# Optimization experiments

Hardware: AMD Instinct MI355X
Metric: run time of the kernel (lower is better)

## Reference

```python
import jax, jax.numpy as jnp
from jax import lax
import numpy as np

EPS = 1e-5  # BatchNorm eps


def setup_inputs() -> dict:
    key = jax.random.key(0)
    ks = jax.random.split(key, 8)
    N, C_in, T, V = 64, 64, 300, 25
    C_out, K, KT = 64, 3, 9
    x = jax.random.normal(ks[0], (N, C_in, T, V), dtype=jnp.float32)
    A = jax.random.uniform(ks[1], (K, V, V), dtype=jnp.float32)
    # 1x1 conv weight squeezed to [K*C_out, C_in]
    w_gcn = jax.random.normal(ks[2], (K * C_out, C_in), dtype=jnp.float32) * (1.0 / np.sqrt(C_in))
    b_gcn = jax.random.normal(ks[3], (K * C_out,), dtype=jnp.float32) * 0.01
    # temporal conv weight [O, I, kT, 1]
    w_tcn = jax.random.normal(ks[4], (C_out, C_out, KT, 1), dtype=jnp.float32) * (1.0 / np.sqrt(C_out * KT))
    b_tcn = jax.random.normal(ks[5], (C_out,), dtype=jnp.float32) * 0.01
    gamma = jnp.ones((C_out,), dtype=jnp.float32)
    beta = jnp.zeros((C_out,), dtype=jnp.float32)
    return {"x": x, "A": A, "w_gcn": w_gcn, "b_gcn": b_gcn,
            "w_tcn": w_tcn, "b_tcn": b_tcn, "gamma": gamma, "beta": beta}


def reference(x, A, w_gcn, b_gcn, w_tcn, b_tcn, gamma, beta):
    K = A.shape[0]
    # unit_gcn: 1x1 conv (pointwise over channels) then spatial graph aggregation
    y = jnp.einsum('nctv,oc->notv', x, w_gcn) + b_gcn[None, :, None, None]  # [N, K*C, T, V]
    n, kc, t, v = y.shape
    y = y.reshape(n, K, kc // K, t, v)
    y = jnp.einsum('nkctv,kvw->nctw', y, A)  # [N, C, T, V]
    # unit_tcn: temporal conv (kernel 9x1, pad 4) + BatchNorm (training mode: batch stats)
    pad = (w_tcn.shape[2] - 1) // 2
    y = lax.conv_general_dilated(y, w_tcn, window_strides=(1, 1),
                                 padding=((pad, pad), (0, 0)),
                                 dimension_numbers=('NCHW', 'OIHW', 'NCHW'))
    y = y + b_tcn[None, :, None, None]
    mean = jnp.mean(y, axis=(0, 2, 3), keepdims=True)
    var = jnp.var(y, axis=(0, 2, 3), keepdims=True)
    y = (y - mean) * lax.rsqrt(var + EPS) * gamma[None, :, None, None] + beta[None, :, None, None]
    # residual (identity: in==out, stride==1) + ReLU
    return jax.nn.relu(y + x)
```

## Files before the change

### kernel.cpp

```cpp
#include <hip/hip_runtime.h>
#include <hip/hip_bf16.h>

#define N_    64
#define C_    64
#define T_    300
#define V_    25
#define K_    3
#define KT_   9
#define PAD_  4

typedef short bf16x8 __attribute__((ext_vector_type(8)));
typedef float f32x4  __attribute__((ext_vector_type(4)));

static __device__ __forceinline__ unsigned short f2bf(float f) {
    __hip_bfloat16 h = __float2bfloat16(f);
    return __builtin_bit_cast(unsigned short, h);
}
static __device__ __forceinline__ unsigned int pk2(float a, float b) {
    return (unsigned int)f2bf(a) | ((unsigned int)f2bf(b) << 16);
}
static __device__ __forceinline__ float bfhi(unsigned int u) {
    return __builtin_bit_cast(float, u << 16);
}
static __device__ __forceinline__ float bflo(unsigned int u) {
    return __builtin_bit_cast(float, u & 0xffff0000u);
}
static __device__ __forceinline__ float bf2f(unsigned short u) {
    return __builtin_bit_cast(float, (unsigned int)u << 16);
}

__global__ __launch_bounds__(256) void prep_kernel(
    const float* __restrict__ Wt, const float* __restrict__ Wg,
    const float* __restrict__ bg, const float* __restrict__ A,
    unsigned short* __restrict__ Wtb, unsigned short* __restrict__ Wgbt,
    unsigned short* __restrict__ bias2b, unsigned short* __restrict__ Abt)
{
    int i = blockIdx.x * 256 + threadIdx.x;
    if (i < 9*64*64) {
        int kt = i >> 12, r = i & 4095, o = r >> 6, c = r & 63;
        Wtb[i] = f2bf(Wt[(size_t)(o*64 + c)*9 + kt]);
    }
    int j = i - 9*64*64;
    if (j >= 0 && j < 64*192) {
        int o = j / 192, kc = j - 192*(j/192);
        int k = kc >> 6, ci = kc & 63;
        Wgbt[j] = f2bf(Wg[(size_t)(k*64 + o)*64 + ci]);
    }
    int m = j - 64*192;
    if (m >= 0 && m < 64*25) {
        int c = m / 25, w = m - 25*(m/25);
        float s = 0.f;
        for (int k = 0; k < 3; ++k) {
            float col = 0.f;
            for (int v = 0; v < 25; ++v) col += A[k*625 + v*25 + w];
            s += bg[k*64 + c] * col;
        }
        bias2b[w*64 + c] = f2bf(s);
    }
    int p = m - 64*25;
    if (p >= 0 && p < 3*32*40) {
        int k = p / 1280, r = p - 1280*k, w = r / 40, v = r - 40*(r/40);
        float val = (w < 25 && v < 25) ? A[k*625 + v*25 + w] : 0.f;
        Abt[p] = f2bf(val);
    }
}

#define GSUB   15
#define GGRP   (T_/GSUB)
#define NGBLK  (N_*GGRP)

__global__ __launch_bounds__(256, 5) void gcn_kernel(
    const float* __restrict__ x,
    const unsigned short* __restrict__ Wgbt,
    const unsigned short* __restrict__ Abt,
    const unsigned short* __restrict__ bias2b,
    unsigned short* __restrict__ y2)
{
    __shared__ unsigned short xslab[64*40];
    __shared__ unsigned short xa[32*200];
    __shared__ unsigned int   bias2L[25*34];

    const int tid  = threadIdx.x;
    const int n    = blockIdx.x / GGRP;
    const int tg   = (blockIdx.x % GGRP) * GSUB;
    const int lane = tid & 63, wave = tid >> 6;
    const int l15  = lane & 15, lq = lane >> 4;

    bf16x8 wfrag[6], afrag[6];
    #pragma unroll
    for (int cb = 0; cb < 6; ++cb) {
        wfrag[cb] = *(const bf16x8*)(Wgbt + (wave*16 + l15)*192 + cb*32 + lq*8);
        asm volatile("" : "+v"(wfrag[cb]));
    }
    #pragma unroll
    for (int s = 0; s < 6; ++s) {
        afrag[s] = *(const bf16x8*)(Abt + ((s >> 1)*32 + (s & 1)*16 + l15)*40 + lq*8);
        asm volatile("" : "+v"(afrag[s]));
    }

    for (int i = tid; i < 800; i += 256)
        bias2L[(i >> 5)*34 + (i & 31)] = ((const unsigned int*)bias2b)[i];
    if (tid < 192) {
        int r = tid / 3, z = tid - 3*(tid/3);
        ((unsigned int*)xslab)[r*20 + 13 + z] = 0u;
    }
    #pragma unroll
    for (int s = 0; s < 4; ++s) {
        int slot = tid + s*256;
        if (slot < 64*13) {
            int row = slot/13, sl = slot - 13*row;
            const float* xr = x + ((size_t)(n*C_ + row)*T_ + tg)*V_;
            float f0, f1;
            if (sl < 12) { float2 t2 = *(const float2*)(xr + 2*sl); f0 = t2.x; f1 = t2.y; }
            else         { f0 = xr[24]; f1 = 0.f; }
            ((unsigned int*)xslab)[row*20 + sl] = pk2(f0, f1);
        }
    }
    __syncthreads();

    for (int j = 0; j < GSUB; ++j) {
        const int t = tg + j;
        float2 Lr[4];
        const bool hn = (j + 1 < GSUB);
        if (hn) {
            #pragma unroll
            for (int s = 0; s < 4; ++s) {
                int slot = tid + s*256;
                if (slot < 64*13) {
                    int row = slot/13, sl = slot - 13*row;
                    const float* xr = x + ((size_t)(n*C_ + row)*T_ + t + 1)*V_;
                    if (sl < 12) Lr[s] = *(const float2*)(xr + 2*sl);
                    else         { Lr[s].x = xr[24]; Lr[s].y = 0.f; }
                }
            }
        }
        {
            bf16x8 xf = *(const bf16x8*)(xslab + (wave*16 + l15)*40 + lq*8);
            #pragma unroll
            for (int s = 0; s < 6; ++s) {
                f32x4 d = {};
                d = __builtin_amdgcn_mfma_f32_16x16x32_bf16(xf, afrag[s], d, 0, 0, 0);
                const int w = (s & 1)*16 + l15;
                if (w < 25) {
                    const int k = s >> 1;
                    unsigned long long pv = (unsigned long long)pk2(d[0], d[1])
                                          | ((unsigned long long)pk2(d[2], d[3]) << 32);
                    *(unsigned long long*)((char*)xa + w*400 + k*128 + wave*32 + lq*8) = pv;
                }
            }
        }
        __syncthreads();
        {
            f32x4 acc0 = {}, acc1 = {};
            #pragma unroll
            for (int cb = 0; cb < 6; ++cb) {
                bf16x8 b0 = *(const bf16x8*)((const char*)xa + l15*400      + cb*64 + lq*16);
                bf16x8 b1 = *(const bf16x8*)((const char*)xa + (16+l15)*400 + cb*64 + lq*16);
                acc0 = __builtin_amdgcn_mfma_f32_16x16x32_bf16(wfrag[cb], b0, acc0, 0, 0, 0);
                acc1 = __builtin_amdgcn_mfma_f32_16x16x32_bf16(wfrag[cb], b1, acc1, 0, 0, 0);
            }
            const int o0 = wave*16 + lq*4;
            {
                const int col = l15;
                unsigned int bu0 = bias2L[col*34 + (o0 >> 1)];
                unsigned int bu1 = bias2L[col*34 + (o0 >> 1) + 1];
                float v0 = acc0[0] + bfhi(bu0), v1 = acc0[1] + bflo(bu0);
                float v2 = acc0[2] + bfhi(bu1), v3 = acc0[3] + bflo(bu1);
                const size_t gcol = ((size_t)n*T_ + t)*V_ + col;
                *(unsigned long long*)(y2 + gcol*64 + o0) =
                      (unsigned long long)pk2(v0, v1)
                    | ((unsigned long long)pk2(v2, v3) << 32);
            }
            if (l15 < 9) {
                const int col = 16 + l15;
                unsigned int bu0 = bias2L[col*34 + (o0 >> 1)];
                unsigned int bu1 = bias2L[col*34 + (o0 >> 1) + 1];
                float v0 = acc1[0] + bfhi(bu0), v1 = acc1[1] + bflo(bu0);
                float v2 = acc1[2] + bfhi(bu1), v3 = acc1[3] + bflo(bu1);
                const size_t gcol = ((size_t)n*T_ + t)*V_ + col;
                *(unsigned long long*)(y2 + gcol*64 + o0) =
                      (unsigned long long)pk2(v0, v1)
                    | ((unsigned long long)pk2(v2, v3) << 32);
            }
        }
        if (hn) {
            #pragma unroll
            for (int s = 0; s < 4; ++s) {
                int slot = tid + s*256;
                if (slot < 64*13) {
                    int row = slot/13, sl = slot - 13*row;
                    ((unsigned int*)xslab)[row*20 + sl] = pk2(Lr[s].x, Lr[s].y);
                }
            }
        }
        __syncthreads();
    }
}

#define TTT    20
#define TCOLS  (TTT*25)
#define SLABC  712
#define TTILES (T_/TTT)
#define NBLK   (N_*TTILES)

#define TLOADA(dst, kt_) { \
    _Pragma("unroll") \
    for (int mt = 0; mt < 4; ++mt) \
        dst[mt] = *(const bf16x8*)(Wtb + (size_t)(kt_)*4096 + (mt*16 + l15)*64 \
                                   + h*32 + lq*8); }

#define TCOMP(a_, kt_) { \
    _Pragma("unroll") \
    for (int nf = 0; nf < 8; ++nf) { \
        int col = colw + nf*16 + l15 + (kt_)*25; \
        bf16x8 b = *(const bf16x8*)((const char*)slab + col*80 + lq*16); \
        _Pragma("unroll") \
        for (int mt = 0; mt < 4; ++mt) \
            acc[mt][nf] = __builtin_amdgcn_mfma_f32_16x16x32_bf16( \
                a_[mt], b, acc[mt][nf], 0, 0, 0); } }

template<int BF>
__global__ __launch_bounds__(256, 2) void tcn_kernel(
    const unsigned short* __restrict__ y2, const unsigned short* __restrict__ Wtb,
    const float* __restrict__ bt,
    unsigned short* __restrict__ y3b, float* __restrict__ y3f,
    float* __restrict__ psum, float* __restrict__ psq)
{
    __shared__ unsigned short slab[SLABC*40];
    __shared__ float s_sum[64], s_sq[64];

    const int tid = threadIdx.x;
    const int n  = blockIdx.x / TTILES;
    const int t0 = (blockIdx.x % TTILES) * TTT;
    const int lane = tid & 63, wave = tid >> 6;
    const int l15 = lane & 15, lq = lane >> 4;
    const int colw = wave * 128;

    if (tid < 64) { s_sum[tid] = 0.f; s_sq[tid] = 0.f; }

    f32x4 acc[4][8] = {};

    #pragma unroll
    for (int h = 0; h < 2; ++h) {
        __syncthreads();
        for (int i = tid; i < SLABC*4; i += 256) {
            int col = i >> 2, ck = i & 3;
            int tl = col / 25, v = col - 25*tl;
            int t = t0 - PAD_ + tl;
            float4 val = {0.f, 0.f, 0.f, 0.f};
            if (t >= 0 && t < T_)
                val = *(const float4*)(y2 + (((size_t)(n*T_ + t)*V_ + v)*64 + h*32 + ck*8));
            *(float4*)((char*)slab + col*80 + ck*16) = val;
        }
        __syncthreads();
        bf16x8 aA[4], aB[4];
        TLOADA(aA, 0);
        #pragma unroll
        for (int kt = 0; kt < 9; ++kt) {
            if ((kt & 1) == 0) {
                if (kt < 8) TLOADA(aB, kt + 1);
                TCOMP(aA, kt);
            } else {
                if (kt < 8) TLOADA(aA, kt + 1);
                TCOMP(aB, kt);
            }
        }
    }

    #pragma unroll
    for (int mt = 0; mt < 4; ++mt) {
        #pragma unroll
        for (int r = 0; r < 4; ++r) {
            const int o = mt*16 + lq*4 + r;
            const float bias = bt[o];
            float ls = 0.f, lsq = 0.f;
            #pragma unroll
            for (int nf = 0; nf < 8; ++nf) {
                int ocol = colw + nf*16 + l15;
                if (ocol < TCOLS) {
                    int tl = ocol / 25, v = ocol - 25*tl;
                    float val = acc[mt][nf][r] + bias;
                    size_t idx = ((size_t)(n*C_ + o)*T_ + t0 + tl)*V_ + v;
                    if (BF) y3b[idx] = f2bf(val);
                    else    y3f[idx] = val;
                    ls += val; lsq += val*val;
                }
            }
            atomicAdd(&s_sum[o], ls);
            atomicAdd(&s_sq[o], lsq);
        }
    }
    __syncthreads();
    if (tid < 64) {
        psum[(size_t)tid*NBLK + blockIdx.x] = s_sum[tid];
        psq [(size_t)tid*NBLK + blockIdx.x] = s_sq [tid];
    }
}

__global__ __launch_bounds__(256) void stats_kernel(
    const float* __restrict__ psum, const float* __restrict__ psq,
    const float* __restrict__ gamma, const float* __restrict__ beta,
    float* __restrict__ sb)
{
    const int o = blockIdx.x;
    const int tid = threadIdx.x;
    float s = 0.f, q = 0.f;
    for (int i = tid; i < NBLK; i += 256) {
        s += psum[(size_t)o*NBLK + i];
        q += psq [(size_t)o*NBLK + i];
    }
    __shared__ float rs[256], rq[256];
    rs[tid] = s; rq[tid] = q;
    __syncthreads();
    for (int off = 128; off > 0; off >>= 1) {
        if (tid < off) { rs[tid] += rs[tid + off]; rq[tid] += rq[tid + off]; }
        __syncthreads();
    }
    if (tid == 0) {
        const float cnt = (float)(N_ * T_ * V_);
        float mean = rs[0] / cnt;
        float var  = rq[0] / cnt - mean * mean;
        float rstd = rsqrtf(var + 1e-5f);
        float sc   = gamma[o] * rstd;
        sb[o]      = sc;
        sb[C_ + o] = beta[o] - mean * sc;
    }
}

__global__ __launch_bounds__(256) void bn_res_relu_bf16_kernel(
    const float* __restrict__ x, const unsigned short* __restrict__ y3b,
    const float* __restrict__ sb, float* __restrict__ out)
{
    const size_t total4 = (size_t)N_ * C_ * T_ * V_ / 4;
    size_t i4 = (size_t)blockIdx.x * 256 + threadIdx.x;
    if (i4 >= total4) return;
    const int c = (int)((i4 / (T_ * V_ / 4)) % C_);
    const float sc = sb[c], sh = sb[C_ + c];
    ushort4 yv = ((const ushort4*)y3b)[i4];
    float4 xv = ((const float4*)x)[i4];
    float4 o;
    o.x = fmaxf(bf2f(yv.x) * sc + sh + xv.x, 0.0f);
    o.y = fmaxf(bf2f(yv.y) * sc + sh + xv.y, 0.0f);
    o.z = fmaxf(bf2f(yv.z) * sc + sh + xv.z, 0.0f);
    o.w = fmaxf(bf2f(yv.w) * sc + sh + xv.w, 0.0f);
    ((float4*)out)[i4] = o;
}

__global__ __launch_bounds__(256) void bn_res_relu_f32_kernel(
    const float* __restrict__ x, const float* __restrict__ sb,
    float* __restrict__ y)
{
    const size_t total4 = (size_t)N_ * C_ * T_ * V_ / 4;
    size_t i4 = (size_t)blockIdx.x * 256 + threadIdx.x;
    if (i4 >= total4) return;
    const int c = (int)((i4 / (T_ * V_ / 4)) % C_);
    const float sc = sb[c], sh = sb[C_ + c];
    float4 yv = ((const float4*)y)[i4];
    float4 xv = ((const float4*)x)[i4];
    float4 o;
    o.x = fmaxf(yv.x * sc + sh + xv.x, 0.0f);
    o.y = fmaxf(yv.y * sc + sh + xv.y, 0.0f);
    o.z = fmaxf(yv.z * sc + sh + xv.z, 0.0f);
    o.w = fmaxf(yv.w * sc + sh + xv.w, 0.0f);
    ((float4*)y)[i4] = o;
}

extern "C" void kernel_launch(void* const* d_in, const int* in_sizes, int n_in,
                              void* d_out, int out_size, void* d_ws, size_t ws_size,
                              hipStream_t stream)
{
    const float* x     = (const float*)d_in[0];
    const float* A     = (const float*)d_in[1];
    const float* wg    = (const float*)d_in[2];
    const float* bg    = (const float*)d_in[3];
    const float* wt    = (const float*)d_in[4];
    const float* bt    = (const float*)d_in[5];
    const float* gamma = (const float*)d_in[6];
    const float* beta  = (const float*)d_in[7];
    float* out = (float*)d_out;

    char* wsb = (char*)d_ws;
    const size_t Y2B   = 61440000;
    const size_t Y3B   = 61440000;
    const size_t TABLE = 2*245760 + 512 + 73728 + 24576 + 3200 + 7680;
    const bool usebf = ws_size >= Y2B + Y3B + TABLE;

    unsigned short* y2  = (unsigned short*)wsb;
    unsigned short* y3b = (unsigned short*)(wsb + Y2B);
    const size_t base2  = usebf ? (Y2B + Y3B) : Y2B;
    float* psum            = (float*)(wsb + base2);
    float* psq             = (float*)(wsb + base2 + 245760);
    float* sb              = (float*)(wsb + base2 + 2*245760);
    unsigned short* Wtb    = (unsigned short*)(wsb + base2 + 2*245760 + 512);
    unsigned short* Wgbt   = (unsigned short*)(wsb + base2 + 2*245760 + 512 + 73728);
    unsigned short* bias2b = (unsigned short*)(wsb + base2 + 2*245760 + 512 + 73728 + 24576);
    unsigned short* Abt    = (unsigned short*)(wsb + base2 + 2*245760 + 512 + 73728 + 24576 + 3200);

    prep_kernel<<<214, 256, 0, stream>>>(wt, wg, bg, A, Wtb, Wgbt, bias2b, Abt);
    gcn_kernel<<<NGBLK, 256, 0, stream>>>(x, Wgbt, Abt, bias2b, y2);
    if (usebf)
        tcn_kernel<1><<<NBLK, 256, 0, stream>>>(y2, Wtb, bt, y3b, out, psum, psq);
    else
        tcn_kernel<0><<<NBLK, 256, 0, stream>>>(y2, Wtb, bt, y3b, out, psum, psq);
    stats_kernel<<<C_, 256, 0, stream>>>(psum, psq, gamma, beta, sb);
    const size_t total4 = (size_t)N_ * C_ * T_ * V_ / 4;
    const int bnblk = (int)((total4 + 255) / 256);
    if (usebf)
        bn_res_relu_bf16_kernel<<<bnblk, 256, 0, stream>>>(x, y3b, sb, out);
    else
        bn_res_relu_f32_kernel<<<bnblk, 256, 0, stream>>>(x, sb, out);
}
```

Measured before the change: 266.6 us.

## Widen tcn blocks to 8 waves and stage bf16 output through LDS

The temporal conv kernel now runs 512 threads, with each wave covering 64 output columns instead of 128, so the accumulator array is half as large and occupancy can rise. In the bf16 path, outputs are written into the shared slab and then copied to global memory as contiguous 32-bit words per channel row, replacing scattered 2-byte stores. The slab load loop also drops the per-element divide and time-bounds check in favour of a precomputed column range. The trade-offs are extra barriers and LDS traffic for the staging, and more threads competing for the same LDS.

```diff
diff --git a/kernel.cpp b/kernel.cpp
--- a/kernel.cpp
+++ b/kernel.cpp
@@ -202,6 +202,7 @@
 #define SLABC  712
 #define TTILES (T_/TTT)
 #define NBLK   (N_*TTILES)
+#define BBSTR  516
 
 #define TLOADA(dst, kt_) { \
     _Pragma("unroll") \
@@ -211,7 +212,7 @@
 
 #define TCOMP(a_, kt_) { \
     _Pragma("unroll") \
-    for (int nf = 0; nf < 8; ++nf) { \
+    for (int nf = 0; nf < 4; ++nf) { \
         int col = colw + nf*16 + l15 + (kt_)*25; \
         bf16x8 b = *(const bf16x8*)((const char*)slab + col*80 + lq*16); \
         _Pragma("unroll") \
@@ -220,7 +221,7 @@
                 a_[mt], b, acc[mt][nf], 0, 0, 0); } }
 
 template<int BF>
-__global__ __launch_bounds__(256, 2) void tcn_kernel(
+__global__ __launch_bounds__(512, 4) void tcn_kernel(
     const unsigned short* __restrict__ y2, const unsigned short* __restrict__ Wtb,
     const float* __restrict__ bt,
     unsigned short* __restrict__ y3b, float* __restrict__ y3f,
@@ -234,22 +235,24 @@
     const int t0 = (blockIdx.x % TTILES) * TTT;
     const int lane = tid & 63, wave = tid >> 6;
     const int l15 = lane & 15, lq = lane >> 4;
-    const int colw = wave * 128;
+    const int colw = wave * 64;
 
     if (tid < 64) { s_sum[tid] = 0.f; s_sq[tid] = 0.f; }
 
-    f32x4 acc[4][8] = {};
+    const int lo = (t0 < PAD_) ? (PAD_ - t0)*V_ : 0;
+    const int hi = (t0 + TTT + PAD_ > T_) ? (T_ + PAD_ - t0)*V_ : SLABC;
+
+    f32x4 acc[4][4] = {};
 
     #pragma unroll
     for (int h = 0; h < 2; ++h) {
         __syncthreads();
-        for (int i = tid; i < SLABC*4; i += 256) {
+        const long gbase = ((long)n*T_*V_ + (long)(t0 - PAD_)*V_)*64 + h*32;
+        for (int i = tid; i < SLABC*4; i += 512) {
             int col = i >> 2, ck = i & 3;
-            int tl = col / 25, v = col - 25*tl;
-            int t = t0 - PAD_ + tl;
             float4 val = {0.f, 0.f, 0.f, 0.f};
-            if (t >= 0 && t < T_)
-                val = *(const float4*)(y2 + (((size_t)(n*T_ + t)*V_ + v)*64 + h*32 + ck*8));
+            if (col >= lo && col < hi)
+                val = *(const float4*)(y2 + gbase + (long)col*64 + ck*8);
             *(float4*)((char*)slab + col*80 + ck*16) = val;
         }
         __syncthreads();
@@ -267,27 +270,65 @@
         }
     }
 
-    #pragma unroll
-    for (int mt = 0; mt < 4; ++mt) {
+    if (BF) {
+        unsigned short* bb = slab;
         #pragma unroll
-        for (int r = 0; r < 4; ++r) {
-            const int o = mt*16 + lq*4 + r;
-            const float bias = bt[o];
-            float ls = 0.f, lsq = 0.f;
-            #pragma unroll
-            for (int nf = 0; nf < 8; ++nf) {
-                int ocol = colw + nf*16 + l15;
-                if (ocol < TCOLS) {
-                    int tl = ocol / 25, v = ocol - 25*tl;
-                    float val = acc[mt][nf][r] + bias;
-                    size_t idx = ((size_t)(n*C_ + o)*T_ + t0 + tl)*V_ + v;
-                    if (BF) y3b[idx] = f2bf(val);
-                    else    y3f[idx] = val;
-                    ls += val; lsq += val*val;
-                }
-            }
-            atomicAdd(&s_sum[o], ls);
-            atomicAdd(&s_sq[o], lsq);
+        for (int H = 0; H < 2; ++H) {
+            __syncthreads();
+            #pragma unroll
+            for (int m2 = 0; m2 < 2; ++m2) {
+                const int mt = H*2 + m2;
+                #pragma unroll
+                for (int r = 0; r < 4; ++r) {
+                    const int o = mt*16 + lq*4 + r;
+                    const float bias = bt[o];
+                    float ls = 0.f, lsq = 0.f;
+                    #pragma unroll
+                    for (int nf = 0; nf < 4; ++nf) {
+                        int col = colw + nf*16 + l15;
+                        float val = acc[mt][nf][r] + bias;
+                        if (col < TCOLS) { ls += val; lsq += val*val; }
+                        bb[(o - H*32)*BBSTR + col] = f2bf(val);
+                    }
+                    atomicAdd(&s_sum[o], ls);
+                    atomicAdd(&s_sq[o], lsq);
+                }
+            }
+            __syncthreads();
+            {
+                const int row = tid >> 4, lane16 = tid & 15;
+                const int o = H*32 + row;
+                const unsigned int* src = (const unsigned int*)(bb + row*BBSTR);
+                unsigned int* dst = (unsigned int*)(y3b
+                    + ((size_t)(n*C_ + o)*T_ + t0)*V_);
+                #pragma unroll
+                for (int jj = 0; jj < 16; ++jj) {
+                    int idx = jj*16 + lane16;
+                    if (idx < 250) dst[idx] = src[idx];
+                }
+            }
+        }
+    } else {
+        #pragma unroll
+        for (int mt = 0; mt < 4; ++mt) {
+            #pragma unroll
+            for (int r = 0; r < 4; ++r) {
+                const int o = mt*16 + lq*4 + r;
+                const float bias = bt[o];
+                float ls = 0.f, lsq = 0.f;
+                #pragma unroll
+                for (int nf = 0; nf < 4; ++nf) {
+                    int ocol = colw + nf*16 + l15;
+                    if (ocol < TCOLS) {
+                        int tl = ocol / 25, v = ocol - 25*tl;
+                        float val = acc[mt][nf][r] + bias;
+                        y3f[((size_t)(n*C_ + o)*T_ + t0 + tl)*V_ + v] = val;
+                        ls += val; lsq += val*val;
+                    }
+                }
+                atomicAdd(&s_sum[o], ls);
+                atomicAdd(&s_sq[o], lsq);
+            }
         }
     }
     __syncthreads();
@@ -399,9 +440,9 @@
     prep_kernel<<<214, 256, 0, stream>>>(wt, wg, bg, A, Wtb, Wgbt, bias2b, Abt);
     gcn_kernel<<<NGBLK, 256, 0, stream>>>(x, Wgbt, Abt, bias2b, y2);
     if (usebf)
-        tcn_kernel<1><<<NBLK, 256, 0, stream>>>(y2, Wtb, bt, y3b, out, psum, psq);
+        tcn_kernel<1><<<NBLK, 512, 0, stream>>>(y2, Wtb, bt, y3b, out, psum, psq);
     else
-        tcn_kernel<0><<<NBLK, 256, 0, stream>>>(y2, Wtb, bt, y3b, out, psum, psq);
+        tcn_kernel<0><<<NBLK, 512, 0, stream>>>(y2, Wtb, bt, y3b, out, psum, psq);
     stats_kernel<<<C_, 256, 0, stream>>>(psum, psq, gamma, beta, sb);
     const size_t total4 = (size_t)N_ * C_ * T_ * V_ / 4;
     const int bnblk = (int)((total4 + 255) / 256);
```

Measured after the change: 342.0 us. 28.3% more time.

## Restructure temporal conv to read y2 directly from global instead of LDS slab

Applied to the files above, without the earlier changes.

The temporal conv kernel no longer stages a padded time slab in shared memory. Each wave reads its B fragments straight from global y2, relying on L1/L2 to serve the nine time-shifted reuses. Bounds checks are confined to edge blocks, and each block covers 256 flattened columns rather than 20 time steps. Per-block stat reduction now uses wave shuffles before the LDS atomics. This trades the LDS fill and barriers for many more global loads.

```diff
diff --git a/kernel.cpp b/kernel.cpp
--- a/kernel.cpp
+++ b/kernel.cpp
@@ -197,103 +197,125 @@
     }
 }
 
-#define TTT    20
-#define TCOLS  (TTT*25)
-#define SLABC  712
-#define TTILES (T_/TTT)
-#define NBLK   (N_*TTILES)
-
-#define TLOADA(dst, kt_) { \
-    _Pragma("unroll") \
-    for (int mt = 0; mt < 4; ++mt) \
-        dst[mt] = *(const bf16x8*)(Wtb + (size_t)(kt_)*4096 + (mt*16 + l15)*64 \
-                                   + h*32 + lq*8); }
-
-#define TCOMP(a_, kt_) { \
-    _Pragma("unroll") \
-    for (int nf = 0; nf < 8; ++nf) { \
-        int col = colw + nf*16 + l15 + (kt_)*25; \
-        bf16x8 b = *(const bf16x8*)((const char*)slab + col*80 + lq*16); \
-        _Pragma("unroll") \
-        for (int mt = 0; mt < 4; ++mt) \
-            acc[mt][nf] = __builtin_amdgcn_mfma_f32_16x16x32_bf16( \
-                a_[mt], b, acc[mt][nf], 0, 0, 0); } }
+#define TCN_COLS (T_*V_)
+#define TCPB     256
+#define TBPN     30
+#define TNBLK    (N_*TBPN)
 
 template<int BF>
-__global__ __launch_bounds__(256, 2) void tcn_kernel(
+__global__ __launch_bounds__(256) void tcn_kernel(
     const unsigned short* __restrict__ y2, const unsigned short* __restrict__ Wtb,
     const float* __restrict__ bt,
     unsigned short* __restrict__ y3b, float* __restrict__ y3f,
     float* __restrict__ psum, float* __restrict__ psq)
 {
-    __shared__ unsigned short slab[SLABC*40];
     __shared__ float s_sum[64], s_sq[64];
 
-    const int tid = threadIdx.x;
-    const int n  = blockIdx.x / TTILES;
-    const int t0 = (blockIdx.x % TTILES) * TTT;
+    const int tid  = threadIdx.x;
+    const int n    = blockIdx.x / TBPN;
+    const int bi   = blockIdx.x % TBPN;
     const int lane = tid & 63, wave = tid >> 6;
-    const int l15 = lane & 15, lq = lane >> 4;
-    const int colw = wave * 128;
+    const int l15  = lane & 15, lq = lane >> 4;
+    const int c0   = bi*TCPB + wave*64;
+    const long nbase = (long)n * TCN_COLS;
+    const bool edge = (bi == 0) || (bi >= 28);
 
     if (tid < 64) { s_sum[tid] = 0.f; s_sq[tid] = 0.f; }
 
-    f32x4 acc[4][8] = {};
-
-    #pragma unroll
-    for (int h = 0; h < 2; ++h) {
-        __syncthreads();
-        for (int i = tid; i < SLABC*4; i += 256) {
-            int col = i >> 2, ck = i & 3;
-            int tl = col / 25, v = col - 25*tl;
-            int t = t0 - PAD_ + tl;
-            float4 val = {0.f, 0.f, 0.f, 0.f};
-            if (t >= 0 && t < T_)
-                val = *(const float4*)(y2 + (((size_t)(n*T_ + t)*V_ + v)*64 + h*32 + ck*8));
-            *(float4*)((char*)slab + col*80 + ck*16) = val;
-        }
-        __syncthreads();
-        bf16x8 aA[4], aB[4];
-        TLOADA(aA, 0);
+    f32x4 acc[4][4] = {};
+
+    if (!edge) {
+        const unsigned short* yb = y2 + (nbase + c0 + l15)*64 + lq*8;
         #pragma unroll
         for (int kt = 0; kt < 9; ++kt) {
-            if ((kt & 1) == 0) {
-                if (kt < 8) TLOADA(aB, kt + 1);
-                TCOMP(aA, kt);
-            } else {
-                if (kt < 8) TLOADA(aA, kt + 1);
-                TCOMP(aB, kt);
-            }
-        }
-    }
+            const int s25 = (kt - 4)*25;
+            #pragma unroll
+            for (int cb = 0; cb < 2; ++cb) {
+                bf16x8 a[4];
+                #pragma unroll
+                for (int mt = 0; mt < 4; ++mt)
+                    a[mt] = *(const bf16x8*)(Wtb + kt*4096 + (mt*16 + l15)*64
+                                             + cb*32 + lq*8);
+                #pragma unroll
+                for (int nf = 0; nf < 4; ++nf) {
+                    bf16x8 b = *(const bf16x8*)(yb + (long)(nf*16 + s25)*64 + cb*32);
+                    #pragma unroll
+                    for (int mt = 0; mt < 4; ++mt)
+                        acc[mt][nf] = __builtin_amdgcn_mfma_f32_16x16x32_bf16(
+                            a[mt], b, acc[mt][nf], 0, 0, 0);
+                }
+            }
+        }
+    } else {
+        const bf16x8 bz = {};
+        #pragma unroll
+        for (int kt = 0; kt < 9; ++kt) {
+            const int s25 = (kt - 4)*25;
+            #pragma unroll
+            for (int cb = 0; cb < 2; ++cb) {
+                bf16x8 a[4];
+                #pragma unroll
+                for (int mt = 0; mt < 4; ++mt)
+                    a[mt] = *(const bf16x8*)(Wtb + kt*4096 + (mt*16 + l15)*64
+                                             + cb*32 + lq*8);
+                #pragma unroll
+                for (int nf = 0; nf < 4; ++nf) {
+                    const int colp = c0 + nf*16 + l15 + s25;
+                    const bool valid = (colp >= 0) && (colp < TCN_COLS);
+                    const long off = valid ? (long)colp : 0;
+                    bf16x8 b = *(const bf16x8*)(y2 + (nbase + off)*64 + cb*32 + lq*8);
+                    if (!valid) b = bz;
+                    #pragma unroll
+                    for (int mt = 0; mt < 4; ++mt)
+                        acc[mt][nf] = __builtin_amdgcn_mfma_f32_16x16x32_bf16(
+                            a[mt], b, acc[mt][nf], 0, 0, 0);
+                }
+            }
+        }
+    }
+
+    float ls[16], lsq[16];
+    #pragma unroll
+    for (int e = 0; e < 16; ++e) { ls[e] = 0.f; lsq[e] = 0.f; }
 
     #pragma unroll
     for (int mt = 0; mt < 4; ++mt) {
         #pragma unroll
         for (int r = 0; r < 4; ++r) {
+            const int e = mt*4 + r;
             const int o = mt*16 + lq*4 + r;
             const float bias = bt[o];
-            float ls = 0.f, lsq = 0.f;
-            #pragma unroll
-            for (int nf = 0; nf < 8; ++nf) {
-                int ocol = colw + nf*16 + l15;
-                if (ocol < TCOLS) {
-                    int tl = ocol / 25, v = ocol - 25*tl;
-                    float val = acc[mt][nf][r] + bias;
-                    size_t idx = ((size_t)(n*C_ + o)*T_ + t0 + tl)*V_ + v;
-                    if (BF) y3b[idx] = f2bf(val);
-                    else    y3f[idx] = val;
-                    ls += val; lsq += val*val;
-                }
-            }
-            atomicAdd(&s_sum[o], ls);
-            atomicAdd(&s_sq[o], lsq);
+            #pragma unroll
+            for (int nf = 0; nf < 4; ++nf) {
+                const int col = c0 + nf*16 + l15;
+                if (col < TCN_COLS) {
+                    const float val = acc[mt][nf][r] + bias;
+                    if (BF) y3b[(size_t)(n*C_ + o)*TCN_COLS + col] = f2bf(val);
+                    else    y3f[(size_t)(n*C_ + o)*TCN_COLS + col] = val;
+                    ls[e] += val; lsq[e] += val*val;
+                }
+            }
+        }
+    }
+
+    __syncthreads();
+    #pragma unroll
+    for (int e = 0; e < 16; ++e) {
+        float a = ls[e], b = lsq[e];
+        a += __shfl_xor(a, 1); a += __shfl_xor(a, 2);
+        a += __shfl_xor(a, 4); a += __shfl_xor(a, 8);
+        b += __shfl_xor(b, 1); b += __shfl_xor(b, 2);
+        b += __shfl_xor(b, 4); b += __shfl_xor(b, 8);
+        if (l15 == 0) {
+            const int o = (e >> 2)*16 + lq*4 + (e & 3);
+            atomicAdd(&s_sum[o], a);
+            atomicAdd(&s_sq[o], b);
         }
     }
     __syncthreads();
     if (tid < 64) {
-        psum[(size_t)tid*NBLK + blockIdx.x] = s_sum[tid];
-        psq [(size_t)tid*NBLK + blockIdx.x] = s_sq [tid];
+        psum[(size_t)tid*TNBLK + blockIdx.x] = s_sum[tid];
+        psq [(size_t)tid*TNBLK + blockIdx.x] = s_sq [tid];
     }
 }
 
@@ -305,9 +327,9 @@
     const int o = blockIdx.x;
     const int tid = threadIdx.x;
     float s = 0.f, q = 0.f;
-    for (int i = tid; i < NBLK; i += 256) {
-        s += psum[(size_t)o*NBLK + i];
-        q += psq [(size_t)o*NBLK + i];
+    for (int i = tid; i < TNBLK; i += 256) {
+        s += psum[(size_t)o*TNBLK + i];
+        q += psq [(size_t)o*TNBLK + i];
     }
     __shared__ float rs[256], rq[256];
     rs[tid] = s; rq[tid] = q;
@@ -382,26 +404,27 @@
     char* wsb = (char*)d_ws;
     const size_t Y2B   = 61440000;
     const size_t Y3B   = 61440000;
-    const size_t TABLE = 2*245760 + 512 + 73728 + 24576 + 3200 + 7680;
+    const size_t PSB   = (size_t)C_ * TNBLK * 4;
+    const size_t TABLE = 2*PSB + 512 + 73728 + 24576 + 3200 + 7680;
     const bool usebf = ws_size >= Y2B + Y3B + TABLE;
 
     unsigned short* y2  = (unsigned short*)wsb;
     unsigned short* y3b = (unsigned short*)(wsb + Y2B);
     const size_t base2  = usebf ? (Y2B + Y3B) : Y2B;
     float* psum            = (float*)(wsb + base2);
-    float* psq             = (float*)(wsb + base2 + 245760);
-    float* sb              = (float*)(wsb + base2 + 2*245760);
-    unsigned short* Wtb    = (unsigned short*)(wsb + base2 + 2*245760 + 512);
-    unsigned short* Wgbt   = (unsigned short*)(wsb + base2 + 2*245760 + 512 + 73728);
-    unsigned short* bias2b = (unsigned short*)(wsb + base2 + 2*245760 + 512 + 73728 + 24576);
-    unsigned short* Abt    = (unsigned short*)(wsb + base2 + 2*245760 + 512 + 73728 + 24576 + 3200);
+    float* psq             = (float*)(wsb + base2 + PSB);
+    float* sb              = (float*)(wsb + base2 + 2*PSB);
+    unsigned short* Wtb    = (unsigned short*)(wsb + base2 + 2*PSB + 512);
+    unsigned short* Wgbt   = (unsigned short*)(wsb + base2 + 2*PSB + 512 + 73728);
+    unsigned short* bias2b = (unsigned short*)(wsb + base2 + 2*PSB + 512 + 73728 + 24576);
+    unsigned short* Abt    = (unsigned short*)(wsb + base2 + 2*PSB + 512 + 73728 + 24576 + 3200);
 
     prep_kernel<<<214, 256, 0, stream>>>(wt, wg, bg, A, Wtb, Wgbt, bias2b, Abt);
     gcn_kernel<<<NGBLK, 256, 0, stream>>>(x, Wgbt, Abt, bias2b, y2);
     if (usebf)
-        tcn_kernel<1><<<NBLK, 256, 0, stream>>>(y2, Wtb, bt, y3b, out, psum, psq);
+        tcn_kernel<1><<<TNBLK, 256, 0, stream>>>(y2, Wtb, bt, y3b, out, psum, psq);
     else
-        tcn_kernel<0><<<NBLK, 256, 0, stream>>>(y2, Wtb, bt, y3b, out, psum, psq);
+        tcn_kernel<0><<<TNBLK, 256, 0, stream>>>(y2, Wtb, bt, y3b, out, psum, psq);
     stats_kernel<<<C_, 256, 0, stream>>>(psum, psq, gamma, beta, sb);
     const size_t total4 = (size_t)N_ * C_ * T_ * V_ / 4;
     const int bnblk = (int)((total4 + 255) / 256);
```

Measured after the change: 341.7 us. +28.2%, slower.
